# Performance work log

Measured on AMD Instinct MI355X. Metric: run time of the kernel, lower is better.

## Reference

```python
import jax, jax.numpy as jnp
import numpy as np

EPS = 1e-5


def hyper_graph_conv(x, elements, W, b):
    """x: [B, C, N] vertex features; elements: [M, 8] vertex ids per hex element.
    Gather 8 vertex features per element, apply Linear(8C -> 8Co) on the
    concatenated features, then scatter-mean the 8 outputs back to vertices.
    Returns [B, Co, N]."""
    B, C, N = x.shape
    M = elements.shape[0]
    Co = W.shape[0] // 8
    g = x[:, :, elements]                      # [B, C, M, 8]
    g = jnp.transpose(g, (0, 2, 3, 1)).reshape(B, M, 8 * C)   # [B, M, 8C]
    h = jnp.einsum('bmk,ok->bmo', g, W) + b    # [B, M, 8Co]
    h = h.reshape(B, M * 8, Co)                # per-(element,corner) vertex outputs
    flat = elements.reshape(-1)                # [M*8]
    out = jnp.zeros((B, N, Co), dtype=x.dtype).at[:, flat, :].add(h)
    cnt = jnp.zeros((N,), dtype=x.dtype).at[flat].add(1.0)
    out = out / jnp.maximum(cnt, 1.0)[None, :, None]
    return jnp.transpose(out, (0, 2, 1))       # [B, Co, N]


def batch_norm(x, gamma, beta):
    # BatchNorm1d in training mode over [B, C, N]: stats over (B, N)
    mean = jnp.mean(x, axis=(0, 2), keepdims=True)
    var = jnp.mean(jnp.square(x - mean), axis=(0, 2), keepdims=True)
    xn = (x - mean) * jax.lax.rsqrt(var + EPS)
    return xn * gamma[None, :, None] + beta[None, :, None]


def setup_inputs() -> dict:
    key = jax.random.key(0)
    ks = jax.random.split(key, 8)
    B, Cin, Cout, N, M = 4, 8, 16, 100000, 98304
    return {
        'x': jax.random.normal(ks[0], (B, Cin, N), dtype=jnp.float32),
        'elements': jax.random.randint(ks[1], (M, 8), 0, N, dtype=jnp.int32),
        'W1': jax.random.normal(ks[2], (8 * Cout, 8 * Cin), dtype=jnp.float32) * (1.0 / np.sqrt(8 * Cin)),
        'b1': jnp.zeros((8 * Cout,), dtype=jnp.float32),
        'gamma1': jnp.ones((Cout,), dtype=jnp.float32),
        'beta1': jnp.zeros((Cout,), dtype=jnp.float32),
        'W2': jax.random.normal(ks[3], (8 * Cout, 8 * Cout), dtype=jnp.float32) * (1.0 / np.sqrt(8 * Cout)),
        'b2': jnp.zeros((8 * Cout,), dtype=jnp.float32),
        'gamma2': jnp.ones((Cout,), dtype=jnp.float32),
        'beta2': jnp.zeros((Cout,), dtype=jnp.float32),
        'Wskip': jax.random.normal(ks[4], (Cout, Cin), dtype=jnp.float32) * (1.0 / np.sqrt(Cin)),
        'bskip': jnp.zeros((Cout,), dtype=jnp.float32),
    }


def reference(x, elements, W1, b1, gamma1, beta1, W2, b2, gamma2, beta2, Wskip, bskip):
    out = hyper_graph_conv(x, elements, W1, b1)        # [B, Cout, N]
    out = jax.nn.relu(batch_norm(out, gamma1, beta1))
    out = hyper_graph_conv(out, elements, W2, b2)      # [B, Cout, N]
    out = batch_norm(out, gamma2, beta2)
    skip = jnp.einsum('bcn,oc->bon', x, Wskip) + bskip[None, :, None]  # Conv1d k=1
    out = jax.nn.relu(out + skip)
    return out
```

## Files before the change

kernel.cpp:

```cpp
#include <hip/hip_runtime.h>

#define NB 4
#define CIN 8
#define CO 16
#define NV 100000
#define NVP 100096
#define NM 98304
#define NPOS (NM*8)
#define NBLK ((NV+255)/256)
#define VPW 14
#define REDB 1786

typedef short s16x8 __attribute__((ext_vector_type(8)));
typedef float f32x4 __attribute__((ext_vector_type(4)));
typedef unsigned short u16;
typedef unsigned int u32;

#define OFF_STAT  800256
#define OFF_ROWS  800640
#define OFF_BSUM  1200768
#define OFF_POS   1202432
#define OFF_XTB   4348160
#define OFF_W1B   10748160
#define OFF_W2B   10764544
#define OFF_MBUF  23597312
#define OFF_HBUF  49197312
#define OFF_CNTR  149860608
#define OFF_BASER (OFF_CNTR + 8*NVP*4)
#define WS_NEED   (OFF_BASER + 8*NVP*4)

static __device__ __forceinline__ u16 f2bf(float f){
  union { float f; u32 u; } v; v.f = f;
  u32 r = v.u + 0x7fffu + ((v.u >> 16) & 1u);
  return (u16)(r >> 16);
}
static __device__ __forceinline__ float bf2f_lo(u32 w){
  union { u32 u; float f; } v; v.u = w << 16; return v.f;
}
static __device__ __forceinline__ float bf2f_hi(u32 w){
  union { u32 u; float f; } v; v.u = w & 0xffff0000u; return v.f;
}
static __device__ __forceinline__ float bf2f16(u16 h){
  union { u32 u; float f; } v; v.u = ((u32)h) << 16; return v.f;
}
static __device__ __forceinline__ u32 pk2(float a, float b){
  return (u32)f2bf(a) | (((u32)f2bf(b)) << 16);
}

__global__ __launch_bounds__(256) void k_xt(const float* __restrict__ x, u16* __restrict__ xtb,
    const float* __restrict__ W1, const float* __restrict__ W2,
    u16* __restrict__ w1b, u16* __restrict__ w2b, float* __restrict__ stat,
    int* __restrict__ cntR)
{
  __shared__ float tile[32][257];
  if (blockIdx.x >= NBLK){
    int b3 = blockIdx.x - NBLK;
    if (b3 == 0 && threadIdx.x < 64) stat[threadIdx.x] = 0.f;
    const int T1 = 128*64, T2 = T1 + 128*128;
    for (int i = b3*256 + threadIdx.x; i < T2; i += 8*256){
      if (i < T1) w1b[i] = f2bf(W1[i]);
      else { int j = i - T1; w2b[j] = f2bf(W2[j]); }
    }
    int4 z = {0,0,0,0};
    int4* c4 = (int4*)cntR;
    const int NC4 = (8*NVP*4)/16;
    for (int q = b3*256 + threadIdx.x; q < NC4; q += 8*256) c4[q] = z;
    return;
  }
  int t = threadIdx.x;
  int v0 = blockIdx.x*256;
  #pragma unroll
  for (int r = 0; r < 32; r++){
    int v = v0 + t;
    tile[r][t] = (v < NV) ? x[(size_t)r*NV + v] : 0.f;
  }
  __syncthreads();
  int v = v0 + t;
  if (v < NV){
    u16 o[32] __attribute__((aligned(16)));
    #pragma unroll
    for (int r = 0; r < 32; r++) o[r] = f2bf(tile[r][t]);
    uint4* dst = (uint4*)(xtb + (size_t)v*32);
    #pragma unroll
    for (int k = 0; k < 4; k++) dst[k] = *(uint4*)(o + k*8);
  }
}

__global__ __launch_bounds__(256) void k_slot(const int* __restrict__ elem,
    int* __restrict__ cntR, int* __restrict__ slot)
{
  int b = blockIdx.x;
  int* myc = cntR + (b & 7)*NVP;
  int i0 = b*768 + threadIdx.x;
  #pragma unroll
  for (int k = 0; k < 3; k++){
    int i = i0 + k*256;
    int v = elem[i];
    slot[i] = atomicAdd(myc + v, 1);
  }
}

__global__ __launch_bounds__(256) void k_scan_a(const int* __restrict__ cntR, int* __restrict__ bsum)
{
  int v = blockIdx.x*256 + threadIdx.x;
  int x = 0;
  if (v < NV){
    #pragma unroll
    for (int r = 0; r < 8; r++) x += cntR[r*NVP + v];
  }
  #pragma unroll
  for (int off = 32; off > 0; off >>= 1) x += __shfl_down(x, off);
  __shared__ int ls[4];
  int wid = threadIdx.x >> 6, lane = threadIdx.x & 63;
  if (lane == 0) ls[wid] = x;
  __syncthreads();
  if (threadIdx.x == 0) bsum[blockIdx.x] = ls[0] + ls[1] + ls[2] + ls[3];
}

__global__ __launch_bounds__(256) void k_scan_c(const int* __restrict__ cntR,
    const int* __restrict__ bsum, int* __restrict__ rows, int* __restrict__ baseR)
{
  int wid = threadIdx.x >> 6, lane = threadIdx.x & 63;
  int v = blockIdx.x*256 + threadIdx.x;
  int cr[8];
  #pragma unroll
  for (int r = 0; r < 8; r++) cr[r] = (v < NV) ? cntR[r*NVP + v] : 0;
  int pre[8]; int x = 0;
  #pragma unroll
  for (int r = 0; r < 8; r++){ pre[r] = x; x += cr[r]; }
  int incl = x;
  #pragma unroll
  for (int off = 1; off <= 32; off <<= 1){
    int y = __shfl_up(incl, off);
    if (lane >= off) incl += y;
  }
  __shared__ int wt[4];
  __shared__ int sbase;
  if (lane == 63) wt[wid] = incl;
  if (threadIdx.x < 64){
    int s = 0;
    for (int i = threadIdx.x; i < blockIdx.x; i += 64) s += bsum[i];
    #pragma unroll
    for (int off = 32; off > 0; off >>= 1) s += __shfl_down(s, off);
    if (threadIdx.x == 0) sbase = s;
  }
  __syncthreads();
  int woff = 0;
  for (int w = 0; w < 4; w++) if (w < wid) woff += wt[w];
  if (v < NV){
    int row0 = sbase + woff + incl - x;
    rows[v] = row0;
    #pragma unroll
    for (int r = 0; r < 8; r++) baseR[r*NVP + v] = row0 + pre[r];
  }
}

__global__ __launch_bounds__(256) void k_pos2(const int* __restrict__ elem,
    const int* __restrict__ baseR, int* __restrict__ pos)
{
  int i4 = blockIdx.x*256 + threadIdx.x;
  int4 e = ((const int4*)elem)[i4];
  int4 s = ((const int4*)pos)[i4];
  int r = ((i4*4)/768) & 7;
  const int* br = baseR + r*NVP;
  int4 p;
  p.x = br[e.x] + s.x;
  p.y = br[e.y] + s.y;
  p.z = br[e.z] + s.z;
  p.w = br[e.w] + s.w;
  ((int4*)pos)[i4] = p;
}

__global__ __launch_bounds__(256) void k_conv1(const int* __restrict__ elem,
    const u16* __restrict__ xtb, const u16* __restrict__ w1b,
    const float* __restrict__ b1, const int* __restrict__ pos, u16* __restrict__ hbuf)
{
  const int lane = threadIdx.x & 63;
  const int col = lane & 15, kg = lane >> 4, b = lane & 3;
  s16x8 wf[8][2];
  #pragma unroll
  for (int j2 = 0; j2 < 8; j2++)
    #pragma unroll
    for (int t = 0; t < 2; t++)
      wf[j2][t] = *(const s16x8*)(w1b + (j2*16 + col)*64 + t*32 + kg*8);
  float bb[8];
  #pragma unroll
  for (int j2 = 0; j2 < 8; j2++) bb[j2] = b1[j2*16 + col];

  int wave = (int)((blockIdx.x*blockDim.x + threadIdx.x) >> 6);
  int g0 = wave, g1 = wave + 12288;
  int ma0 = g0*4 + (col >> 2), ma1 = g1*4 + (col >> 2);
  int me0 = g0*4 + kg,         me1 = g1*4 + kg;

  int e00 = elem[ma0*8 + kg], e01 = elem[ma0*8 + 4 + kg];
  int e10 = elem[ma1*8 + kg], e11 = elem[ma1*8 + 4 + kg];
  int4 p0l = *(const int4*)(pos + me0*8), p0h = *(const int4*)(pos + me0*8 + 4);
  int4 p1l = *(const int4*)(pos + me1*8), p1h = *(const int4*)(pos + me1*8 + 4);
  s16x8 a00 = *(const s16x8*)(xtb + (size_t)e00*32 + b*8);
  s16x8 a01 = *(const s16x8*)(xtb + (size_t)e01*32 + b*8);
  s16x8 a10 = *(const s16x8*)(xtb + (size_t)e10*32 + b*8);
  s16x8 a11 = *(const s16x8*)(xtb + (size_t)e11*32 + b*8);

  int pe0[8] = {p0l.x,p0l.y,p0l.z,p0l.w,p0h.x,p0h.y,p0h.z,p0h.w};
  int pe1[8] = {p1l.x,p1l.y,p1l.z,p1l.w,p1h.x,p1h.y,p1h.z,p1h.w};

  #pragma unroll
  for (int j2 = 0; j2 < 8; j2++){
    f32x4 c = {0.f,0.f,0.f,0.f};
    c = __builtin_amdgcn_mfma_f32_16x16x32_bf16(a00, wf[j2][0], c, 0, 0, 0);
    c = __builtin_amdgcn_mfma_f32_16x16x32_bf16(a01, wf[j2][1], c, 0, 0, 0);
    uint2 d; d.x = pk2(c[0]+bb[j2], c[1]+bb[j2]); d.y = pk2(c[2]+bb[j2], c[3]+bb[j2]);
    *(uint2*)(hbuf + (size_t)pe0[j2]*64 + col*4) = d;
  }
  #pragma unroll
  for (int j2 = 0; j2 < 8; j2++){
    f32x4 c = {0.f,0.f,0.f,0.f};
    c = __builtin_amdgcn_mfma_f32_16x16x32_bf16(a10, wf[j2][0], c, 0, 0, 0);
    c = __builtin_amdgcn_mfma_f32_16x16x32_bf16(a11, wf[j2][1], c, 0, 0, 0);
    uint2 d; d.x = pk2(c[0]+bb[j2], c[1]+bb[j2]); d.y = pk2(c[2]+bb[j2], c[3]+bb[j2]);
    *(uint2*)(hbuf + (size_t)pe1[j2]*64 + col*4) = d;
  }
}

__global__ __launch_bounds__(256) void k_conv2(const int* __restrict__ elem,
    const u16* __restrict__ mbuf, const u16* __restrict__ w2b,
    const float* __restrict__ b2, const float* __restrict__ stat,
    const float* __restrict__ gamma, const float* __restrict__ beta,
    const int* __restrict__ pos, u16* __restrict__ hbuf)
{
  __shared__ u16 wl[16384];
  __shared__ float sc[16], sh[16];
  #pragma unroll
  for (int r = 0; r < 8; r++){
    int q = threadIdx.x + 256*r;
    int j2t = q >> 6, ln = q & 63;
    int cc = ln & 15, kk = ln >> 4;
    int j2 = j2t >> 2, tt = j2t & 3;
    *(s16x8*)(wl + (size_t)q*8) =
        *(const s16x8*)(w2b + (j2*16 + cc)*128 + tt*32 + kk*8);
  }
  if (threadIdx.x < 16){
    int co = threadIdx.x;
    const float invn = 1.0f / (float)(NB*NV);
    float m = stat[co]*invn;
    float var = stat[16+co]*invn - m*m;
    float s = gamma[co]*rsqrtf(var + 1e-5f);
    sc[co] = s; sh[co] = beta[co] - m*s;
  }

  const int lane = threadIdx.x & 63;
  const int col = lane & 15, kg = lane >> 4, b = lane & 3;
  const int p = kg >> 1;
  const int c0 = (kg & 1)*8;
  float bb[8];
  #pragma unroll
  for (int j2 = 0; j2 < 8; j2++) bb[j2] = b2[j2*16 + col];

  int wave = (int)((blockIdx.x*blockDim.x + threadIdx.x) >> 6);
  int g0 = wave, g1 = wave + 12288;
  int ma0 = g0*4 + (col >> 2), ma1 = g1*4 + (col >> 2);
  int me0 = g0*4 + kg,         me1 = g1*4 + kg;

  int4 e0l = *(const int4*)(elem + ma0*8), e0h = *(const int4*)(elem + ma0*8 + 4);
  int4 e1l = *(const int4*)(elem + ma1*8), e1h = *(const int4*)(elem + ma1*8 + 4);
  int4 p0l = *(const int4*)(pos + me0*8),  p0h = *(const int4*)(pos + me0*8 + 4);
  int4 p1l = *(const int4*)(pos + me1*8),  p1h = *(const int4*)(pos + me1*8 + 4);

  int v00 = p ? e0l.y : e0l.x, v01 = p ? e0l.w : e0l.z;
  int v02 = p ? e0h.y : e0h.x, v03 = p ? e0h.w : e0h.z;
  int v10 = p ? e1l.y : e1l.x, v11 = p ? e1l.w : e1l.z;
  int v12 = p ? e1h.y : e1h.x, v13 = p ? e1h.w : e1h.z;

  s16x8 af0[4], af1[4];
  af0[0] = *(const s16x8*)(mbuf + (size_t)v00*64 + b*16 + c0);
  af0[1] = *(const s16x8*)(mbuf + (size_t)v01*64 + b*16 + c0);
  af0[2] = *(const s16x8*)(mbuf + (size_t)v02*64 + b*16 + c0);
  af0[3] = *(const s16x8*)(mbuf + (size_t)v03*64 + b*16 + c0);
  af1[0] = *(const s16x8*)(mbuf + (size_t)v10*64 + b*16 + c0);
  af1[1] = *(const s16x8*)(mbuf + (size_t)v11*64 + b*16 + c0);
  af1[2] = *(const s16x8*)(mbuf + (size_t)v12*64 + b*16 + c0);
  af1[3] = *(const s16x8*)(mbuf + (size_t)v13*64 + b*16 + c0);

  int pe0[8] = {p0l.x,p0l.y,p0l.z,p0l.w,p0h.x,p0h.y,p0h.z,p0h.w};
  int pe1[8] = {p1l.x,p1l.y,p1l.z,p1l.w,p1h.x,p1h.y,p1h.z,p1h.w};

  __syncthreads();

  #pragma unroll
  for (int t = 0; t < 4; t++){
    u32 r0[4], r1[4];
    #pragma unroll
    for (int ii = 0; ii < 4; ii++){
      int ca = c0 + 2*ii, cb = ca + 1;
      float x0 = bf2f16((u16)af0[t][2*ii])   * sc[ca] + sh[ca];
      float x1 = bf2f16((u16)af0[t][2*ii+1]) * sc[cb] + sh[cb];
      float y0 = bf2f16((u16)af1[t][2*ii])   * sc[ca] + sh[ca];
      float y1 = bf2f16((u16)af1[t][2*ii+1]) * sc[cb] + sh[cb];
      r0[ii] = pk2(fmaxf(x0, 0.f), fmaxf(x1, 0.f));
      r1[ii] = pk2(fmaxf(y0, 0.f), fmaxf(y1, 0.f));
    }
    af0[t] = *(s16x8*)r0;
    af1[t] = *(s16x8*)r1;
  }

  #pragma unroll
  for (int j2 = 0; j2 < 8; j2++){
    s16x8 w0 = *(const s16x8*)(wl + ((size_t)(j2*4 + 0)*64 + lane)*8);
    s16x8 w1 = *(const s16x8*)(wl + ((size_t)(j2*4 + 1)*64 + lane)*8);
    s16x8 w2 = *(const s16x8*)(wl + ((size_t)(j2*4 + 2)*64 + lane)*8);
    s16x8 w3 = *(const s16x8*)(wl + ((size_t)(j2*4 + 3)*64 + lane)*8);
    f32x4 c = {0.f,0.f,0.f,0.f};
    c = __builtin_amdgcn_mfma_f32_16x16x32_bf16(af0[0], w0, c, 0, 0, 0);
    c = __builtin_amdgcn_mfma_f32_16x16x32_bf16(af0[1], w1, c, 0, 0, 0);
    c = __builtin_amdgcn_mfma_f32_16x16x32_bf16(af0[2], w2, c, 0, 0, 0);
    c = __builtin_amdgcn_mfma_f32_16x16x32_bf16(af0[3], w3, c, 0, 0, 0);
    uint2 d; d.x = pk2(c[0]+bb[j2], c[1]+bb[j2]); d.y = pk2(c[2]+bb[j2], c[3]+bb[j2]);
    *(uint2*)(hbuf + (size_t)pe0[j2]*64 + col*4) = d;
  }
  #pragma unroll
  for (int j2 = 0; j2 < 8; j2++){
    s16x8 w0 = *(const s16x8*)(wl + ((size_t)(j2*4 + 0)*64 + lane)*8);
    s16x8 w1 = *(const s16x8*)(wl + ((size_t)(j2*4 + 1)*64 + lane)*8);
    s16x8 w2 = *(const s16x8*)(wl + ((size_t)(j2*4 + 2)*64 + lane)*8);
    s16x8 w3 = *(const s16x8*)(wl + ((size_t)(j2*4 + 3)*64 + lane)*8);
    f32x4 c = {0.f,0.f,0.f,0.f};
    c = __builtin_amdgcn_mfma_f32_16x16x32_bf16(af1[0], w0, c, 0, 0, 0);
    c = __builtin_amdgcn_mfma_f32_16x16x32_bf16(af1[1], w1, c, 0, 0, 0);
    c = __builtin_amdgcn_mfma_f32_16x16x32_bf16(af1[2], w2, c, 0, 0, 0);
    c = __builtin_amdgcn_mfma_f32_16x16x32_bf16(af1[3], w3, c, 0, 0, 0);
    uint2 d; d.x = pk2(c[0]+bb[j2], c[1]+bb[j2]); d.y = pk2(c[2]+bb[j2], c[3]+bb[j2]);
    *(uint2*)(hbuf + (size_t)pe1[j2]*64 + col*4) = d;
  }
}

__global__ __launch_bounds__(256) void k_reduce(const u16* __restrict__ hbuf,
    const int* __restrict__ rows, u16* __restrict__ mbuf, float* __restrict__ stat)
{
  int lane = threadIdx.x & 63, wid = threadIdx.x >> 6;
  int half = lane >> 5;
  int hl   = lane & 31;
  int k8   = lane & 7;
  int rg   = (lane >> 3) & 3;
  int w = (blockIdx.x*blockDim.x + threadIdx.x) >> 6;
  int v0 = w * VPW;

  int vv = v0 + lane;
  int rr = 0;
  if (lane < VPW + 1) rr = (vv < NV) ? rows[vv] : NPOS;

  int rs[7], ce[7];
  #pragma unroll
  for (int j = 0; j < 7; j++){
    rs[j] = __shfl(rr, 2*j + half);
    ce[j] = __shfl(rr, 2*j + half + 1) - rs[j];
  }

  uint4 d0[7], d1[7], d2[7];
  #pragma unroll
  for (int j = 0; j < 7; j++){
    uint4 z = {0u,0u,0u,0u};
    d0[j] = z; d1[j] = z; d2[j] = z;
    const u16* base = hbuf + (size_t)rs[j]*64 + hl*8;
    if (rg     < ce[j]) d0[j] = *(const uint4*)(base);
    if (4 + rg < ce[j]) d1[j] = *(const uint4*)(base + 4*64);
    if (8 + rg < ce[j]) d2[j] = *(const uint4*)(base + 8*64);
  }

  float st_s0 = 0.f, st_q0 = 0.f, st_s1 = 0.f, st_q1 = 0.f;

  #pragma unroll
  for (int j = 0; j < 7; j++){
    float a0,a1,a2,a3,a4,a5,a6,a7;
    {
      uint4 dA = d0[j], dB = d1[j], dC = d2[j];
      a0 = bf2f_lo(dA.x)+bf2f_lo(dB.x)+bf2f_lo(dC.x);
      a1 = bf2f_hi(dA.x)+bf2f_hi(dB.x)+bf2f_hi(dC.x);
      a2 = bf2f_lo(dA.y)+bf2f_lo(dB.y)+bf2f_lo(dC.y);
      a3 = bf2f_hi(dA.y)+bf2f_hi(dB.y)+bf2f_hi(dC.y);
      a4 = bf2f_lo(dA.z)+bf2f_lo(dB.z)+bf2f_lo(dC.z);
      a5 = bf2f_hi(dA.z)+bf2f_hi(dB.z)+bf2f_hi(dC.z);
      a6 = bf2f_lo(dA.w)+bf2f_lo(dB.w)+bf2f_lo(dC.w);
      a7 = bf2f_hi(dA.w)+bf2f_hi(dB.w)+bf2f_hi(dC.w);
    }
    for (int p = 12; p < ce[j]; p += 4){
      uint4 d = {0u,0u,0u,0u};
      if (p + rg < ce[j]) d = *(const uint4*)(hbuf + (size_t)(rs[j]+p)*64 + hl*8);
      a0 += bf2f_lo(d.x); a1 += bf2f_hi(d.x); a2 += bf2f_lo(d.y); a3 += bf2f_hi(d.y);
      a4 += bf2f_lo(d.z); a5 += bf2f_hi(d.z); a6 += bf2f_lo(d.w); a7 += bf2f_hi(d.w);
    }
    #pragma unroll
    for (int off = 8; off <= 16; off <<= 1){
      a0 += __shfl_xor(a0, off); a1 += __shfl_xor(a1, off);
      a2 += __shfl_xor(a2, off); a3 += __shfl_xor(a3, off);
      a4 += __shfl_xor(a4, off); a5 += __shfl_xor(a5, off);
      a6 += __shfl_xor(a6, off); a7 += __shfl_xor(a7, off);
    }
    int v = v0 + 2*j + half;
    if (hl < 8 && v < NV){
      float inv = 1.0f / fmaxf((float)ce[j], 1.0f);
      float c0b[4] = {a0*inv, a1*inv, a2*inv, a3*inv};
      float c1b[4] = {a4*inv, a5*inv, a6*inv, a7*inv};
      #pragma unroll
      for (int q = 0; q < 4; q++){
        *(u32*)(mbuf + (size_t)v*64 + q*16 + 2*k8) = pk2(c0b[q], c1b[q]);
        st_s0 += c0b[q]; st_q0 += c0b[q]*c0b[q];
        st_s1 += c1b[q]; st_q1 += c1b[q]*c1b[q];
      }
    }
  }

  st_s0 += __shfl_xor(st_s0, 32); st_q0 += __shfl_xor(st_q0, 32);
  st_s1 += __shfl_xor(st_s1, 32); st_q1 += __shfl_xor(st_q1, 32);
  __shared__ float ls[4][16], lq[4][16];
  if (lane < 8){
    ls[wid][2*k8] = st_s0; ls[wid][2*k8+1] = st_s1;
    lq[wid][2*k8] = st_q0; lq[wid][2*k8+1] = st_q1;
  }
  __syncthreads();
  if (threadIdx.x < 32){
    int c2 = threadIdx.x & 15, which = threadIdx.x >> 4;
    float tot = 0.f;
    #pragma unroll
    for (int w2 = 0; w2 < 4; w2++) tot += which ? lq[w2][c2] : ls[w2][c2];
    unsafeAtomicAdd(stat + which*16 + c2, tot);
  }
}

__global__ __launch_bounds__(256) void k_final(const u16* __restrict__ mbuf,
    const float* __restrict__ stat, const float* __restrict__ gamma,
    const float* __restrict__ beta, const float* __restrict__ x,
    const float* __restrict__ wsk, const float* __restrict__ bsk, float* __restrict__ out)
{
  __shared__ float sc[16], sh[16];
  if (threadIdx.x < 16){
    int co = threadIdx.x;
    const float invn = 1.0f / (float)(NB*NV);
    float m = stat[co]*invn;
    float var = stat[16+co]*invn - m*m;
    float s = gamma[co]*rsqrtf(var + 1e-5f);
    sc[co] = s; sh[co] = beta[co] - m*s + bsk[co];
  }
  __syncthreads();
  int n = blockIdx.x*blockDim.x + threadIdx.x;
  int b = blockIdx.y;
  if (n >= NV) return;
  float xv[8];
  #pragma unroll
  for (int c = 0; c < 8; c++) xv[c] = x[((size_t)b*8 + c)*NV + n];
  const uint4* src = (const uint4*)(mbuf + (size_t)n*64 + b*16);
  uint4 m0 = src[0], m1 = src[1];
  u32 mw[8] = {m0.x,m0.y,m0.z,m0.w,m1.x,m1.y,m1.z,m1.w};
  #pragma unroll
  for (int k = 0; k < 8; k++){
    #pragma unroll
    for (int h = 0; h < 2; h++){
      int co = 2*k + h;
      float val = (h ? bf2f_hi(mw[k]) : bf2f_lo(mw[k]))*sc[co] + sh[co];
      #pragma unroll
      for (int c = 0; c < 8; c++) val += wsk[co*8+c]*xv[c];
      out[((size_t)b*16 + co)*NV + n] = fmaxf(val, 0.f);
    }
  }
}

extern "C" void kernel_launch(void* const* d_in, const int* in_sizes, int n_in,
                              void* d_out, int out_size, void* d_ws, size_t ws_size,
                              hipStream_t stream) {
  const float* x    = (const float*)d_in[0];
  const int*   elem = (const int*)  d_in[1];
  const float* W1   = (const float*)d_in[2];
  const float* b1   = (const float*)d_in[3];
  const float* g1   = (const float*)d_in[4];
  const float* be1  = (const float*)d_in[5];
  const float* W2   = (const float*)d_in[6];
  const float* b2   = (const float*)d_in[7];
  const float* g2   = (const float*)d_in[8];
  const float* be2  = (const float*)d_in[9];
  const float* Wsk  = (const float*)d_in[10];
  const float* bsk  = (const float*)d_in[11];
  float* out = (float*)d_out;

  if (ws_size < (size_t)WS_NEED) return;

  char* ws = (char*)d_ws;
  float* stat  = (float*)(ws + OFF_STAT);
  int*   rows  = (int*)  (ws + OFF_ROWS);
  int*   bsum  = (int*)  (ws + OFF_BSUM);
  int*   pos   = (int*)  (ws + OFF_POS);
  u16*   xtb   = (u16*)  (ws + OFF_XTB);
  u16*   w1b   = (u16*)  (ws + OFF_W1B);
  u16*   w2b   = (u16*)  (ws + OFF_W2B);
  u16*   mbuf  = (u16*)  (ws + OFF_MBUF);
  u16*   hbuf  = (u16*)  (ws + OFF_HBUF);
  int*   cntR  = (int*)  (ws + OFF_CNTR);
  int*   baseR = (int*)  (ws + OFF_BASER);

  k_xt<<<NBLK + 8, 256, 0, stream>>>(x, xtb, W1, W2, w1b, w2b, stat, cntR);
  k_slot<<<1024, 256, 0, stream>>>(elem, cntR, pos);
  k_scan_a<<<NBLK, 256, 0, stream>>>(cntR, bsum);
  k_scan_c<<<NBLK, 256, 0, stream>>>(cntR, bsum, rows, baseR);
  k_pos2<<<768, 256, 0, stream>>>(elem, baseR, pos);

  k_conv1<<<3072, 256, 0, stream>>>(elem, xtb, w1b, b1, pos, hbuf);
  k_reduce<<<REDB, 256, 0, stream>>>(hbuf, rows, mbuf, stat);

  k_conv2<<<3072, 256, 0, stream>>>(elem, mbuf, w2b, b2, stat, g1, be1, pos, hbuf);
  k_reduce<<<REDB, 256, 0, stream>>>(hbuf, rows, mbuf, stat + 32);
  k_final<<<dim3((NV+255)/256, NB), 256, 0, stream>>>(mbuf, stat + 32, g2, be2, x, Wsk, bsk, out);
}
```

Baseline: 225.0 us.

## Fuse CSR scan and position kernels into one cooperative kernel with grid syncs

Merges the two scan kernels and the position-fixup kernel into a single cooperative launch that uses grid-wide syncs between the phases. This removes two kernel launches and their implicit barriers, and the block-sum pass now reuses the per-vertex counts already loaded instead of reading cntR twice. The cost is the grid.sync overhead and the need for all 391 blocks to be co-resident. The pos phase also runs with fewer threads in a strided loop.

```diff
diff --git a/kernel.cpp b/kernel.cpp
--- a/kernel.cpp
+++ b/kernel.cpp
@@ -1,4 +1,7 @@
 #include <hip/hip_runtime.h>
+#include <hip/hip_cooperative_groups.h>
+
+namespace cg = cooperative_groups;
 
 #define NB 4
 #define CIN 8
@@ -100,28 +103,14 @@
   }
 }
 
-__global__ __launch_bounds__(256) void k_scan_a(const int* __restrict__ cntR, int* __restrict__ bsum)
-{
-  int v = blockIdx.x*256 + threadIdx.x;
-  int x = 0;
-  if (v < NV){
-    #pragma unroll
-    for (int r = 0; r < 8; r++) x += cntR[r*NVP + v];
-  }
-  #pragma unroll
-  for (int off = 32; off > 0; off >>= 1) x += __shfl_down(x, off);
-  __shared__ int ls[4];
-  int wid = threadIdx.x >> 6, lane = threadIdx.x & 63;
-  if (lane == 0) ls[wid] = x;
-  __syncthreads();
-  if (threadIdx.x == 0) bsum[blockIdx.x] = ls[0] + ls[1] + ls[2] + ls[3];
-}
-
-__global__ __launch_bounds__(256) void k_scan_c(const int* __restrict__ cntR,
-    const int* __restrict__ bsum, int* __restrict__ rows, int* __restrict__ baseR)
-{
+__global__ __launch_bounds__(256) void k_csr(const int* __restrict__ elem,
+    const int* __restrict__ cntR, int* __restrict__ bsum,
+    int* __restrict__ rows, int* __restrict__ baseR, int* __restrict__ pos)
+{
+  cg::grid_group grid = cg::this_grid();
   int wid = threadIdx.x >> 6, lane = threadIdx.x & 63;
   int v = blockIdx.x*256 + threadIdx.x;
+
   int cr[8];
   #pragma unroll
   for (int r = 0; r < 8; r++) cr[r] = (v < NV) ? cntR[r*NVP + v] : 0;
@@ -135,40 +124,45 @@
     if (lane >= off) incl += y;
   }
   __shared__ int wt[4];
-  __shared__ int sbase;
+  __shared__ int sbase_s;
   if (lane == 63) wt[wid] = incl;
+  __syncthreads();
+  if (threadIdx.x == 0) bsum[blockIdx.x] = wt[0] + wt[1] + wt[2] + wt[3];
+
+  grid.sync();
+
   if (threadIdx.x < 64){
     int s = 0;
     for (int i = threadIdx.x; i < blockIdx.x; i += 64) s += bsum[i];
     #pragma unroll
     for (int off = 32; off > 0; off >>= 1) s += __shfl_down(s, off);
-    if (threadIdx.x == 0) sbase = s;
+    if (threadIdx.x == 0) sbase_s = s;
   }
   __syncthreads();
   int woff = 0;
   for (int w = 0; w < 4; w++) if (w < wid) woff += wt[w];
   if (v < NV){
-    int row0 = sbase + woff + incl - x;
+    int row0 = sbase_s + woff + incl - x;
     rows[v] = row0;
     #pragma unroll
     for (int r = 0; r < 8; r++) baseR[r*NVP + v] = row0 + pre[r];
   }
-}
-
-__global__ __launch_bounds__(256) void k_pos2(const int* __restrict__ elem,
-    const int* __restrict__ baseR, int* __restrict__ pos)
-{
-  int i4 = blockIdx.x*256 + threadIdx.x;
-  int4 e = ((const int4*)elem)[i4];
-  int4 s = ((const int4*)pos)[i4];
-  int r = ((i4*4)/768) & 7;
-  const int* br = baseR + r*NVP;
-  int4 p;
-  p.x = br[e.x] + s.x;
-  p.y = br[e.y] + s.y;
-  p.z = br[e.z] + s.z;
-  p.w = br[e.w] + s.w;
-  ((int4*)pos)[i4] = p;
+
+  grid.sync();
+
+  const int stride = NBLK*256;
+  for (int i4 = blockIdx.x*256 + threadIdx.x; i4 < NPOS/4; i4 += stride){
+    int4 e = ((const int4*)elem)[i4];
+    int4 s = ((const int4*)pos)[i4];
+    int r = ((i4*4)/768) & 7;
+    const int* br = baseR + r*NVP;
+    int4 p;
+    p.x = br[e.x] + s.x;
+    p.y = br[e.y] + s.y;
+    p.z = br[e.z] + s.z;
+    p.w = br[e.w] + s.w;
+    ((int4*)pos)[i4] = p;
+  }
 }
 
 __global__ __launch_bounds__(256) void k_conv1(const int* __restrict__ elem,
@@ -497,9 +491,14 @@
 
   k_xt<<<NBLK + 8, 256, 0, stream>>>(x, xtb, W1, W2, w1b, w2b, stat, cntR);
   k_slot<<<1024, 256, 0, stream>>>(elem, cntR, pos);
-  k_scan_a<<<NBLK, 256, 0, stream>>>(cntR, bsum);
-  k_scan_c<<<NBLK, 256, 0, stream>>>(cntR, bsum, rows, baseR);
-  k_pos2<<<768, 256, 0, stream>>>(elem, baseR, pos);
+
+  {
+    const int* elem_a = elem; const int* cntR_a = cntR;
+    int* bsum_a = bsum; int* rows_a = rows; int* baseR_a = baseR; int* pos_a = pos;
+    void* args[] = {(void*)&elem_a, (void*)&cntR_a, (void*)&bsum_a,
+                    (void*)&rows_a, (void*)&baseR_a, (void*)&pos_a};
+    hipLaunchCooperativeKernel((const void*)k_csr, dim3(NBLK), dim3(256), args, 0, stream);
+  }
 
   k_conv1<<<3072, 256, 0, stream>>>(elem, xtb, w1b, b1, pos, hbuf);
   k_reduce<<<REDB, 256, 0, stream>>>(hbuf, rows, mbuf, stat);
```

Result: slower. 307.5 us (+36.6%).
